# Optimization experiments

Hardware: AMD Instinct MI355X
Metric: run time of the kernel (lower is better)

## Reference

```python
import jax, jax.numpy as jnp
import numpy as np
from jax import lax


def setup_inputs() -> dict:
    key = jax.random.key(0)
    ks = jax.random.split(key, 20)
    B, T, Fin = 64, 360, 4
    C, H, W = 128, 32, 32          # encoder_hidden_dim, map size
    D, Hs, Ws = 128, 8, 8          # encoder_downsampled_dim, att feature map
    E, Hd, A, IF, O = 32, 128, 64, 128, 5
    IN = IF + C + E                # LSTMCell input size = 288
    s = 0.05
    # xy coords in [0, 0.31) so floor(v*100) is a valid index < 32
    prev_output_tokens = jax.random.uniform(ks[0], (B, T, Fin)) * 0.31 + 0.001
    feature = jax.random.normal(ks[1], (B, C, H, W))
    final_hidden = jax.random.normal(ks[2], (B, D, Hs, Ws))
    inp = dict(
        prev_output_tokens=prev_output_tokens,
        feature=feature,
        final_hidden=final_hidden,
        W_embed=jax.random.normal(ks[3], (Fin, E)) * s,
        b_embed=jnp.zeros((E,)),
        W_ih=jax.random.normal(ks[4], (IN, 4 * Hd)) * s,
        b_ih=jnp.zeros((4 * Hd,)),
        W_hh=jax.random.normal(ks[5], (Hd, 4 * Hd)) * s,
        b_hh=jnp.zeros((4 * Hd,)),
        W_h2att=jax.random.normal(ks[6], (Hd, A)) * s,
        b_h2att=jnp.zeros((A,)),
        W_alpha=jax.random.normal(ks[7], (A, 1)) * s,
        b_alpha=jnp.zeros((1,)),
        W_encproj=jax.random.normal(ks[8], (D, A)) * s,
        b_encproj=jnp.zeros((A,)),
        W_aap=jax.random.normal(ks[9], (Hd + D, IF)) * s,
        b_aap=jnp.zeros((IF,)),
        W_out=jax.random.normal(ks[10], (IF, O)) * s,
        b_out=jnp.zeros((O,)),
    )
    return inp


def reference(prev_output_tokens, feature, final_hidden,
              W_embed, b_embed, W_ih, b_ih, W_hh, b_hh,
              W_h2att, b_h2att, W_alpha, b_alpha,
              W_encproj, b_encproj, W_aap, b_aap, W_out, b_out):
    B, T, _ = prev_output_tokens.shape
    C, H = feature.shape[1], feature.shape[2]
    D = final_hidden.shape[1]
    Hd = W_hh.shape[0]
    IF = W_aap.shape[1]

    # embed_tokens (Linear)
    x_emb = prev_output_tokens @ W_embed + b_embed          # [B,T,E]

    # xy gather indices: floor(v*100), flat = y*H + x (torch uses size(-2))
    xy = (prev_output_tokens[..., :2] * 100).astype(jnp.int32)
    xy = jnp.where(xy == -1, 0, xy)
    idx = xy[..., 1] * H + xy[..., 0]                       # [B,T]
    feat_flat = feature.reshape(B, C, -1)                   # [B,C,H*W]

    # attention features and their projection (precomputed, as in torch)
    enc_feats = final_hidden.reshape(B, D, -1).transpose(0, 2, 1)   # [B,S,D]
    p_enc = enc_feats @ W_encproj + b_encproj                        # [B,S,A]

    def step(carry, xs):
        h, c, in_feed = carry
        xj, idxj = xs                                       # [B,E], [B]
        # gather encoder feature at the token's xy position
        in_seq = jnp.take_along_axis(feat_flat, idxj[:, None, None], axis=2)[..., 0]  # [B,C]
        inp = jnp.concatenate([xj, in_seq, in_feed], axis=-1)          # [B,288]
        # LSTMCell (torch gate order i,f,g,o)
        gates = inp @ W_ih + b_ih + h @ W_hh + b_hh
        i, f, g, o = jnp.split(gates, 4, axis=-1)
        c = jax.nn.sigmoid(f) * c + jax.nn.sigmoid(i) * jnp.tanh(g)
        h = jax.nn.sigmoid(o) * jnp.tanh(c)
        # additive attention
        att_h = h @ W_h2att + b_h2att                        # [B,A]
        dot = jnp.tanh(p_enc + att_h[:, None, :])            # [B,S,A]
        scores = (dot @ W_alpha)[..., 0] + b_alpha[0]        # [B,S]
        wgt = jax.nn.softmax(scores, axis=1)
        att_res = jnp.einsum('bs,bsd->bd', wgt, enc_feats)   # [B,D]
        out = jnp.concatenate([h, att_res], axis=-1) @ W_aap + b_aap  # [B,IF]
        return (h, c, out), out

    carry0 = (jnp.zeros((B, Hd), x_emb.dtype),
              jnp.zeros((B, Hd), x_emb.dtype),
              jnp.zeros((B, IF), x_emb.dtype))
    xs = (x_emb.transpose(1, 0, 2), idx.T)
    _, outs = lax.scan(step, carry0, xs)                     # [T,B,IF]
    x = outs.transpose(1, 0, 2)                              # [B,T,IF]
    return x @ W_out + b_out                                 # [B,T,5]
```

## Files before the change

### kernel.cpp

```cpp
#include <hip/hip_runtime.h>
#include <hip/hip_bf16.h>

#define BDIM 64
#define TDIM 360
#define BT (BDIM*TDIM)
#define CDIM 128
#define HWSZ 1024
#define SDIM 64
#define G4 512
#define KTOP 160

typedef __hip_bfloat16 bf16;

static __device__ __forceinline__ unsigned int f2bu(float x) {
    bf16 b = __float2bfloat16(x);
    unsigned short u; __builtin_memcpy(&u, &b, 2); return (unsigned int)u;
}
static __device__ __forceinline__ float b2f(bf16 x) { return __bfloat162float(x); }
static __device__ __forceinline__ float bl(unsigned int u) { return __uint_as_float(u << 16); }
static __device__ __forceinline__ float bh(unsigned int u) { return __uint_as_float(u & 0xffff0000u); }
static __device__ __forceinline__ float tanh_fast(float x) {
    float e = __expf(2.0f * x);
    return 1.0f - 2.0f / (e + 1.0f);
}
static __device__ __forceinline__ float sigm(float x) {
    return 1.0f / (1.0f + __expf(-x));
}

__device__ float        g_ArowsF[BT * KTOP];
__device__ float        g_pre2[BT * G4];
__device__ __align__(16) unsigned int g_wpk2[16 * 1024 * 4];
__device__ float        g_wrecA[128 * G4];
__device__ __align__(16) unsigned int g_encW2[BDIM * G4 * 32];
__device__ float        g_encWao[BDIM * 64 * 5];
__device__ float        g_penc[BDIM * SDIM * 64];
__device__ float        g_hw[BT * 192];
__device__ float        g_Wao[256 * 5];
__device__ float        g_bao[5];
__device__ float        g_bias[G4];
__device__ float        g_c0[G4];

__global__ void kA1(const float* __restrict__ tok, const float* __restrict__ feat,
                    const float* __restrict__ Wemb, const float* __restrict__ bemb) {
    int row  = blockIdx.x * 4 + (threadIdx.x >> 6);
    int lane = threadIdx.x & 63;
    const float* tp = tok + (size_t)row * 4;
    float t0 = tp[0], t1 = tp[1], t2 = tp[2], t3 = tp[3];
    int b = row / TDIM;
    int x = (int)(t0 * 100.0f);
    int y = (int)(t1 * 100.0f);
    x = min(max(x, 0), 31);
    y = min(max(y, 0), 31);
    int idx = y * 32 + x;
    float* out = g_ArowsF + (size_t)row * KTOP;
    if (lane < 32) {
        float e = t0 * Wemb[lane] + t1 * Wemb[32 + lane] +
                  t2 * Wemb[64 + lane] + t3 * Wemb[96 + lane] + bemb[lane];
        out[lane] = e;
    }
    const float* fb = feat + (size_t)b * CDIM * HWSZ + idx;
    out[32 + lane]      = fb[(size_t)lane * HWSZ];
    out[32 + 64 + lane] = fb[(size_t)(64 + lane) * HWSZ];
}

__global__ void kA2a(const float* __restrict__ Wih, const float* __restrict__ Whh,
                     const float* __restrict__ Waap) {
    __shared__ float sa0[128], sa1[128];
    int p = blockIdx.x, n = threadIdx.x;
    int r0 = 2 * p, r1 = 2 * p + 1;
    if (n < 128)            sa0[n]        = Waap[r0 * 128 + n];
    else if (n < 256)       sa1[n - 128]  = Waap[r1 * 128 + (n - 128)];
    __syncthreads();
    float acc0 = (r0 < 128) ? Whh[r0 * G4 + n] : 0.0f;
    float acc1 = (r1 < 128) ? Whh[r1 * G4 + n] : 0.0f;
    for (int j = 0; j < 128; ++j) {
        float wi = Wih[(160 + j) * G4 + n];
        acc0 += sa0[j] * wi;
        acc1 += sa1[j] * wi;
    }
    int kh = p >> 6, j = p & 63;
    int jblk = j >> 2, jj = j & 3;
    int u = kh * 512 + n;
    g_wpk2[((size_t)jblk * 1024 + u) * 4 + jj] = f2bu(acc0) | (f2bu(acc1) << 16);
    if (p >= 64) {
        g_wrecA[(r0 - 128) * G4 + n] = acc0;
        g_wrecA[(r1 - 128) * G4 + n] = acc1;
    }
}

__global__ void kA2c(const float* __restrict__ bih, const float* __restrict__ bhh,
                     const float* __restrict__ Wih, const float* __restrict__ Waap,
                     const float* __restrict__ baap, const float* __restrict__ Wout,
                     const float* __restrict__ bout) {
    __shared__ float sb[128];
    int n = threadIdx.x;
    if (n < 128) sb[n] = baap[n];
    __syncthreads();
    g_bias[n] = bih[n] + bhh[n];
    float c0 = 0.0f;
    for (int j = 0; j < 128; ++j) c0 += sb[j] * Wih[(160 + j) * G4 + n];
    g_c0[n] = c0;
    if (n < 256) {
        for (int o = 0; o < 5; ++o) {
            float acc = 0.0f;
            for (int j = 0; j < 128; ++j) acc += Waap[n * 128 + j] * Wout[j * 5 + o];
            g_Wao[n * 5 + o] = acc;
        }
    }
    if (n == 0) {
        for (int o = 0; o < 5; ++o) {
            float acc = bout[o];
            for (int j = 0; j < 128; ++j) acc += sb[j] * Wout[j * 5 + o];
            g_bao[o] = acc;
        }
    }
}

__global__ void kA2d(const float* __restrict__ FH, const float* __restrict__ Wep,
                     const float* __restrict__ bep) {
    __shared__ float sfh[128 * 64];
    int b = blockIdx.x, tid = threadIdx.x;
    for (int i = tid; i < 128 * 64; i += 256) sfh[i] = FH[(size_t)b * 128 * 64 + i];
    __syncthreads();
    int a = tid & 63, sg = tid >> 6;
    float bias = bep[a];
    float acc[16];
#pragma unroll
    for (int i = 0; i < 16; ++i) acc[i] = bias;
    for (int d = 0; d < 128; ++d) {
        float wa = Wep[d * 64 + a];
#pragma unroll
        for (int i = 0; i < 16; ++i) acc[i] += sfh[d * 64 + sg * 16 + i] * wa;
    }
    for (int i = 0; i < 16; ++i)
        g_penc[((size_t)b * 64 + sg * 16 + i) * 64 + a] = acc[i];
}

__global__ void kA2e(const float* __restrict__ FH) {
    __shared__ float encL[64][129];
    int b = blockIdx.x, tid = threadIdx.x;
    for (int i = tid; i < 8192; i += 512) {
        int d = i >> 6, s = i & 63;
        encL[s][d] = FH[(size_t)b * 8192 + i];
    }
    __syncthreads();
    int n = tid;
#pragma unroll 1
    for (int sc = 0; sc < 8; ++sc) {
        float acc[8];
#pragma unroll
        for (int j = 0; j < 8; ++j) acc[j] = 0.f;
        for (int d = 0; d < 128; ++d) {
            float wv = g_wrecA[d * G4 + n];
#pragma unroll
            for (int j = 0; j < 8; ++j) acc[j] += encL[sc * 8 + j][d] * wv;
        }
#pragma unroll
        for (int j = 0; j < 4; ++j) {
            int s2 = sc * 4 + j;
            g_encW2[((size_t)b * G4 + n) * 32 + s2] =
                f2bu(acc[2 * j]) | (f2bu(acc[2 * j + 1]) << 16);
        }
    }
    if (tid < 64) {
        for (int o = 0; o < 5; ++o) {
            float acc = 0.f;
            for (int d = 0; d < 128; ++d)
                acc += encL[tid][d] * g_Wao[(128 + d) * 5 + o];
            g_encWao[((size_t)b * 64 + tid) * 5 + o] = acc;
        }
    }
}

__global__ void __attribute__((amdgpu_flat_work_group_size(512, 512),
                               amdgpu_waves_per_eu(2, 2)))
kB(const float* __restrict__ Wih) {
    int n = threadIdx.x;
    int m0 = blockIdx.x * 8;
    int pl = ((n & 127) << 2) | (n >> 7);
    float racc[8];
#pragma unroll
    for (int r = 0; r < 8; ++r) racc[r] = 0.0f;
#pragma unroll 1
    for (int pass = 0; pass < 2; ++pass) {
        float wcol[80];
#pragma unroll
        for (int j = 0; j < 80; ++j) wcol[j] = Wih[(pass * 80 + j) * G4 + n];
#pragma unroll
        for (int r = 0; r < 8; ++r) {
            const float4* rp = (const float4*)(g_ArowsF + (size_t)(m0 + r) * KTOP + pass * 80);
            float a0 = 0.f, a1 = 0.f, a2 = 0.f, a3 = 0.f;
#pragma unroll
            for (int q = 0; q < 20; ++q) {
                float4 v = rp[q];
                a0 += wcol[4 * q + 0] * v.x;
                a1 += wcol[4 * q + 1] * v.y;
                a2 += wcol[4 * q + 2] * v.z;
                a3 += wcol[4 * q + 3] * v.w;
            }
            racc[r] += (a0 + a1) + (a2 + a3);
        }
    }
#pragma unroll
    for (int r = 0; r < 8; ++r)
        g_pre2[(size_t)(m0 + r) * G4 + pl] = racc[r];
}

#define CONS1(W, jb) { \
    float4 v0 = vals[2 * (jb)], v1 = vals[2 * (jb) + 1]; \
    acc0 += bl(W.x) * v0.x;  acc1 += bh(W.x) * v0.y; \
    acc0 += bl(W.y) * v0.z;  acc1 += bh(W.y) * v0.w; \
    acc0 += bl(W.z) * v1.x;  acc1 += bh(W.z) * v1.y; \
    acc0 += bl(W.w) * v1.z;  acc1 += bh(W.w) * v1.w; }
#define LDP(R, jb)  R = wp[(jb) * 1024];

#define SYNC() do { __builtin_amdgcn_sched_barrier(0); \
    asm volatile("s_waitcnt lgkmcnt(0)" ::: "memory"); \
    __builtin_amdgcn_s_barrier(); \
    __builtin_amdgcn_sched_barrier(0); } while (0)

__global__ void __launch_bounds__(512) kC(const float* __restrict__ Walpha,
                                          const float* __restrict__ balpha,
                                          const float* __restrict__ bh2a,
                                          const float* __restrict__ W2a) {
    __shared__ __align__(16) float s_h[128];
    __shared__ __align__(16) float s_atth[64];
    __shared__ float s_scores[64];
    __shared__ __align__(8)  float s_wgt[64];
    __shared__ float s_walpha[64];
    __shared__ float s_bh2a[64];
    extern __shared__ __align__(16) char dsm[];
    unsigned int* s_encW = (unsigned int*)dsm;
    float* s_penc = (float*)(dsm + 69632);
    bf16*  s_w2aT = (bf16*)(dsm + 69632 + 16640);

    int tid = threadIdx.x;
    int b = blockIdx.x;
    int lane = tid & 63;
    int qb = lane & ~3;
    int n = ((tid & 3) << 7) | (tid >> 2);
    int m = tid >> 2;

    const uint4* wp = ((const uint4*)g_wpk2) + n;
    uint4 P0,P1,P2,P3,P4,P5,P6,P7,P8,P9,P10,P11,P12,P13,P14,P15;
    LDP(P0,0)  LDP(P1,1)  LDP(P2,2)  LDP(P3,3)
    LDP(P4,4)  LDP(P5,5)  LDP(P6,6)  LDP(P7,7)
    LDP(P8,8)  LDP(P9,9)  LDP(P10,10) LDP(P11,11)
    LDP(P12,12) LDP(P13,13) LDP(P14,14) LDP(P15,15)

    float bias_r = g_bias[n];
    float bc_r   = bias_r + g_c0[n];
    float c_reg  = 0.0f;

    if (tid < 128) s_h[tid] = 0.0f;
    if (tid < 64) { s_walpha[tid] = Walpha[tid]; s_bh2a[tid] = bh2a[tid]; }
    for (int i = tid; i < 16384; i += 512) {
        int row = i >> 5, s2 = i & 31;
        int loc = ((row & 127) << 2) | (row >> 7);
        s_encW[loc * 34 + s2] = g_encW2[(size_t)b * 16384 + i];
    }
    for (int i = tid; i < 4096; i += 512) {
        int s = i >> 6, a = i & 63;
        s_penc[s * 65 + a] = g_penc[((size_t)b * 64 + s) * 64 + a];
    }
    for (int i = tid; i < 8192; i += 512) {
        int d = i >> 6, s = i & 63;
        s_w2aT[s * 136 + d] = __float2bfloat16(W2a[i]);
    }
    float bal = balpha[0];

    const float* pre2p = g_pre2 + (size_t)b * TDIM * G4 + tid;
    float* hwp0 = g_hw + (size_t)b * TDIM * 192;

    for (int t = 0; t < TDIM; ++t) {
        SYNC();
        float pre2v = pre2p[(size_t)t * G4];
        float acc0 = 0.f, acc1 = 0.f;
        const float4* vals = (const float4*)s_h;
        CONS1(P0,0)  CONS1(P1,1)  CONS1(P2,2)  CONS1(P3,3)
        CONS1(P4,4)  CONS1(P5,5)  CONS1(P6,6)  CONS1(P7,7)
        CONS1(P8,8)  CONS1(P9,9)  CONS1(P10,10) CONS1(P11,11)
        CONS1(P12,12) CONS1(P13,13) CONS1(P14,14) CONS1(P15,15)
        float g = acc0 + acc1 + pre2v + (t ? bc_r : bias_r);
        if (t) {
            const uint2* er = (const uint2*)(s_encW + tid * 34);
            const float2* wg2 = (const float2*)s_wgt;
            float w0 = 0.f, w1 = 0.f;
#pragma unroll
            for (int j = 0; j < 16; ++j) {
                uint2 ew = er[j];
                float2 wa = wg2[2 * j], wb = wg2[2 * j + 1];
                w0 += bl(ew.x) * wa.x;  w1 += bh(ew.x) * wa.y;
                w0 += bl(ew.y) * wb.x;  w1 += bh(ew.y) * wb.y;
            }
            g += w0 + w1;
        }
        {
            float gi = __shfl(g, qb + 0);
            float gf = __shfl(g, qb + 1);
            float gg = __shfl(g, qb + 2);
            float go = __shfl(g, qb + 3);
            float c = sigm(gf) * c_reg + sigm(gi) * tanh_fast(gg);
            c_reg = c;
            float h = sigm(go) * tanh_fast(c);
            if ((tid & 3) == 0) {
                s_h[m] = h;
                hwp0[(size_t)t * 192 + m] = h;
            }
        }
        SYNC();
        {
            int a = tid >> 3, sub = tid & 7;
            const float4* hv4 = (const float4*)s_h;
            float4 h0 = hv4[4 * sub], h1 = hv4[4 * sub + 1],
                   h2 = hv4[4 * sub + 2], h3 = hv4[4 * sub + 3];
            uint4 w0 = *(const uint4*)&s_w2aT[a * 136 + 16 * sub];
            uint4 w1 = *(const uint4*)&s_w2aT[a * 136 + 16 * sub + 8];
            float acc = bl(w0.x) * h0.x + bh(w0.x) * h0.y +
                        bl(w0.y) * h0.z + bh(w0.y) * h0.w +
                        bl(w0.z) * h1.x + bh(w0.z) * h1.y +
                        bl(w0.w) * h1.z + bh(w0.w) * h1.w +
                        bl(w1.x) * h2.x + bh(w1.x) * h2.y +
                        bl(w1.y) * h2.z + bh(w1.y) * h2.w +
                        bl(w1.z) * h3.x + bh(w1.z) * h3.y +
                        bl(w1.w) * h3.z + bh(w1.w) * h3.w;
            acc += __shfl_xor(acc, 1);
            acc += __shfl_xor(acc, 2);
            acc += __shfl_xor(acc, 4);
            if (sub == 0) s_atth[a] = acc + s_bh2a[a];
        }
        SYNC();
        {
            int ss = tid >> 3, sub = tid & 7;
            float acc = 0.f;
#pragma unroll
            for (int j = 0; j < 8; ++j) {
                int a = sub * 8 + j;
                float xv = s_penc[ss * 65 + a] + s_atth[a];
                acc += tanh_fast(xv) * s_walpha[a];
            }
            acc += __shfl_xor(acc, 1);
            acc += __shfl_xor(acc, 2);
            acc += __shfl_xor(acc, 4);
            if (sub == 0) s_scores[ss] = acc + bal;
        }
        SYNC();
        if (tid < 64) {
            float v = s_scores[tid];
            float mx = v;
#pragma unroll
            for (int off = 32; off > 0; off >>= 1) mx = fmaxf(mx, __shfl_xor(mx, off));
            float e = __expf(v - mx);
            float sum = e;
#pragma unroll
            for (int off = 32; off > 0; off >>= 1) sum += __shfl_xor(sum, off);
            float w = e / sum;
            s_wgt[tid] = w;
            hwp0[(size_t)t * 192 + 128 + tid] = w;
        }
    }
}

__global__ void kD(float* __restrict__ out) {
    int r = blockIdx.x * 4 + (threadIdx.x >> 6);
    int lane = threadIdx.x & 63;
    int b = r / TDIM;
    float acc[5] = {0.f, 0.f, 0.f, 0.f, 0.f};
    if (lane < 48) {
        const float4* hv = (const float4*)(g_hw + (size_t)r * 192);
        float4 v = hv[lane];
        int k0 = lane * 4;
        if (lane < 32) {
#pragma unroll
            for (int o = 0; o < 5; ++o)
                acc[o] = v.x * g_Wao[(k0 + 0) * 5 + o] + v.y * g_Wao[(k0 + 1) * 5 + o] +
                         v.z * g_Wao[(k0 + 2) * 5 + o] + v.w * g_Wao[(k0 + 3) * 5 + o];
        } else {
            int s0 = k0 - 128;
            const float* ew = g_encWao + ((size_t)b * 64 + s0) * 5;
#pragma unroll
            for (int o = 0; o < 5; ++o)
                acc[o] = v.x * ew[o] + v.y * ew[5 + o] + v.z * ew[10 + o] + v.w * ew[15 + o];
        }
    }
#pragma unroll
    for (int off = 32; off > 0; off >>= 1) {
#pragma unroll
        for (int o = 0; o < 5; ++o) acc[o] += __shfl_xor(acc[o], off);
    }
    if (lane == 0) {
#pragma unroll
        for (int o = 0; o < 5; ++o) out[(size_t)r * 5 + o] = acc[o] + g_bao[o];
    }
}

extern "C" void kernel_launch(void* const* d_in, const int* in_sizes, int n_in,
                              void* d_out, int out_size, void* d_ws, size_t ws_size,
                              hipStream_t stream) {
    (void)in_sizes; (void)n_in; (void)d_ws; (void)ws_size; (void)out_size;
    const float* tok  = (const float*)d_in[0];
    const float* feat = (const float*)d_in[1];
    const float* FH   = (const float*)d_in[2];
    const float* Wemb = (const float*)d_in[3];
    const float* bemb = (const float*)d_in[4];
    const float* Wih  = (const float*)d_in[5];
    const float* bih  = (const float*)d_in[6];
    const float* Whh  = (const float*)d_in[7];
    const float* bhh  = (const float*)d_in[8];
    const float* W2a  = (const float*)d_in[9];
    const float* bh2a = (const float*)d_in[10];
    const float* Wal  = (const float*)d_in[11];
    const float* bal  = (const float*)d_in[12];
    const float* Wep  = (const float*)d_in[13];
    const float* bep  = (const float*)d_in[14];
    const float* Waap = (const float*)d_in[15];
    const float* baap = (const float*)d_in[16];
    const float* Wout = (const float*)d_in[17];
    const float* bout = (const float*)d_in[18];
    float* out = (float*)d_out;

    const int kc_dyn_lds = 69632 + 16640 + 17408;
    (void)hipFuncSetAttribute((const void*)kC,
                              hipFuncAttributeMaxDynamicSharedMemorySize,
                              kc_dyn_lds);

    kA1<<<dim3(BT / 4), dim3(256), 0, stream>>>(tok, feat, Wemb, bemb);
    kA2a<<<dim3(128), dim3(512), 0, stream>>>(Wih, Whh, Waap);
    kA2c<<<dim3(1), dim3(512), 0, stream>>>(bih, bhh, Wih, Waap, baap, Wout, bout);
    kA2d<<<dim3(64), dim3(256), 0, stream>>>(FH, Wep, bep);
    kA2e<<<dim3(BDIM), dim3(512), 0, stream>>>(FH);
    kB<<<dim3(BT / 8), dim3(512), 0, stream>>>(Wih);
    kC<<<dim3(64), dim3(512), kc_dyn_lds, stream>>>(Wal, bal, bh2a, W2a);
    kD<<<dim3(BT / 4), dim3(256), 0, stream>>>(out);
}
```

Measured before the change: 1.459 ms.

## Switch recurrent matvecs to packed fp16 with v_dot2 instructions

Converts the packed recurrent weights, per-batch encoder weights, and h2att weights from bf16 to fp16 pairs. Hidden state and attention weights are also stored in shared memory as packed fp16 pairs. Inner products then use the fdot2 intrinsic, which does two multiply-adds per instruction, instead of unpacking bf16 and running scalar FMAs. This cuts ALU work and LDS traffic on the serial per-timestep critical path. In exchange, fp16 range and precision limits apply, the conversion uses round-toward-zero, and cross-lane shuffles are added to build the packed pairs.

Measured after the change: 1.328 ms. 1.1x faster.

```diff
diff --git a/kernel.cpp b/kernel.cpp
--- a/kernel.cpp
+++ b/kernel.cpp
@@ -11,14 +11,24 @@
 #define KTOP 160
 
 typedef __hip_bfloat16 bf16;
+typedef __fp16 h2 __attribute__((ext_vector_type(2)));
 
 static __device__ __forceinline__ unsigned int f2bu(float x) {
     bf16 b = __float2bfloat16(x);
     unsigned short u; __builtin_memcpy(&u, &b, 2); return (unsigned int)u;
 }
-static __device__ __forceinline__ float b2f(bf16 x) { return __bfloat162float(x); }
 static __device__ __forceinline__ float bl(unsigned int u) { return __uint_as_float(u << 16); }
 static __device__ __forceinline__ float bh(unsigned int u) { return __uint_as_float(u & 0xffff0000u); }
+static __device__ __forceinline__ h2 u2h(unsigned int u) {
+    h2 r; __builtin_memcpy(&r, &u, 4); return r;
+}
+static __device__ __forceinline__ unsigned int packh(float a, float b) {
+    h2 v = __builtin_amdgcn_cvt_pkrtz(a, b);
+    unsigned int u; __builtin_memcpy(&u, &v, 4); return u;
+}
+static __device__ __forceinline__ float fdot2(unsigned int a, unsigned int b, float c) {
+    return __builtin_amdgcn_fdot2(u2h(a), u2h(b), c, false);
+}
 static __device__ __forceinline__ float tanh_fast(float x) {
     float e = __expf(2.0f * x);
     return 1.0f - 2.0f / (e + 1.0f);
@@ -81,7 +91,7 @@
     int kh = p >> 6, j = p & 63;
     int jblk = j >> 2, jj = j & 3;
     int u = kh * 512 + n;
-    g_wpk2[((size_t)jblk * 1024 + u) * 4 + jj] = f2bu(acc0) | (f2bu(acc1) << 16);
+    g_wpk2[((size_t)jblk * 1024 + u) * 4 + jj] = packh(acc0, acc1);
     if (p >= 64) {
         g_wrecA[(r0 - 128) * G4 + n] = acc0;
         g_wrecA[(r1 - 128) * G4 + n] = acc1;
@@ -158,8 +168,7 @@
 #pragma unroll
         for (int j = 0; j < 4; ++j) {
             int s2 = sc * 4 + j;
-            g_encW2[((size_t)b * G4 + n) * 32 + s2] =
-                f2bu(acc[2 * j]) | (f2bu(acc[2 * j + 1]) << 16);
+            g_encW2[((size_t)b * G4 + n) * 32 + s2] = packh(acc[2 * j], acc[2 * j + 1]);
         }
     }
     if (tid < 64) {
@@ -206,12 +215,11 @@
         g_pre2[(size_t)(m0 + r) * G4 + pl] = racc[r];
 }
 
-#define CONS1(W, jb) { \
-    float4 v0 = vals[2 * (jb)], v1 = vals[2 * (jb) + 1]; \
-    acc0 += bl(W.x) * v0.x;  acc1 += bh(W.x) * v0.y; \
-    acc0 += bl(W.y) * v0.z;  acc1 += bh(W.y) * v0.w; \
-    acc0 += bl(W.z) * v1.x;  acc1 += bh(W.z) * v1.y; \
-    acc0 += bl(W.w) * v1.z;  acc1 += bh(W.w) * v1.w; }
+#define CONS1f(W, jb) { uint4 hp = hvals4[jb]; \
+    acc0 = fdot2(W.x, hp.x, acc0); \
+    acc1 = fdot2(W.y, hp.y, acc1); \
+    acc0 = fdot2(W.z, hp.z, acc0); \
+    acc1 = fdot2(W.w, hp.w, acc1); }
 #define LDP(R, jb)  R = wp[(jb) * 1024];
 
 #define SYNC() do { __builtin_amdgcn_sched_barrier(0); \
@@ -223,16 +231,16 @@
                                           const float* __restrict__ balpha,
                                           const float* __restrict__ bh2a,
                                           const float* __restrict__ W2a) {
-    __shared__ __align__(16) float s_h[128];
+    __shared__ __align__(16) unsigned int s_h2[64];
     __shared__ __align__(16) float s_atth[64];
     __shared__ float s_scores[64];
-    __shared__ __align__(8)  float s_wgt[64];
-    __shared__ float s_walpha[64];
+    __shared__ __align__(16) unsigned int s_wgt2[32];
+    __shared__ __align__(16) float s_walpha[64];
     __shared__ float s_bh2a[64];
     extern __shared__ __align__(16) char dsm[];
-    unsigned int* s_encW = (unsigned int*)dsm;
-    float* s_penc = (float*)(dsm + 69632);
-    bf16*  s_w2aT = (bf16*)(dsm + 69632 + 16640);
+    unsigned int* s_encW  = (unsigned int*)dsm;
+    float*        s_penc  = (float*)(dsm + 69632);
+    unsigned int* s_w2aTp = (unsigned int*)(dsm + 69632 + 16640);
 
     int tid = threadIdx.x;
     int b = blockIdx.x;
@@ -252,8 +260,7 @@
     float bc_r   = bias_r + g_c0[n];
     float c_reg  = 0.0f;
 
-    if (tid < 128) s_h[tid] = 0.0f;
-    if (tid < 64) { s_walpha[tid] = Walpha[tid]; s_bh2a[tid] = bh2a[tid]; }
+    if (tid < 64) { s_h2[tid] = 0u; s_walpha[tid] = Walpha[tid]; s_bh2a[tid] = bh2a[tid]; }
     for (int i = tid; i < 16384; i += 512) {
         int row = i >> 5, s2 = i & 31;
         int loc = ((row & 127) << 2) | (row >> 7);
@@ -263,9 +270,9 @@
         int s = i >> 6, a = i & 63;
         s_penc[s * 65 + a] = g_penc[((size_t)b * 64 + s) * 64 + a];
     }
-    for (int i = tid; i < 8192; i += 512) {
-        int d = i >> 6, s = i & 63;
-        s_w2aT[s * 136 + d] = __float2bfloat16(W2a[i]);
+    for (int i = tid; i < 4096; i += 512) {
+        int a = i & 63, k2 = i >> 6;
+        s_w2aTp[a * 68 + k2] = packh(W2a[(2 * k2) * 64 + a], W2a[(2 * k2 + 1) * 64 + a]);
     }
     float bal = balpha[0];
 
@@ -276,22 +283,21 @@
         SYNC();
         float pre2v = pre2p[(size_t)t * G4];
         float acc0 = 0.f, acc1 = 0.f;
-        const float4* vals = (const float4*)s_h;
-        CONS1(P0,0)  CONS1(P1,1)  CONS1(P2,2)  CONS1(P3,3)
-        CONS1(P4,4)  CONS1(P5,5)  CONS1(P6,6)  CONS1(P7,7)
-        CONS1(P8,8)  CONS1(P9,9)  CONS1(P10,10) CONS1(P11,11)
-        CONS1(P12,12) CONS1(P13,13) CONS1(P14,14) CONS1(P15,15)
+        const uint4* hvals4 = (const uint4*)s_h2;
+        CONS1f(P0,0)  CONS1f(P1,1)  CONS1f(P2,2)  CONS1f(P3,3)
+        CONS1f(P4,4)  CONS1f(P5,5)  CONS1f(P6,6)  CONS1f(P7,7)
+        CONS1f(P8,8)  CONS1f(P9,9)  CONS1f(P10,10) CONS1f(P11,11)
+        CONS1f(P12,12) CONS1f(P13,13) CONS1f(P14,14) CONS1f(P15,15)
         float g = acc0 + acc1 + pre2v + (t ? bc_r : bias_r);
         if (t) {
             const uint2* er = (const uint2*)(s_encW + tid * 34);
-            const float2* wg2 = (const float2*)s_wgt;
+            const uint2* wg = (const uint2*)s_wgt2;
             float w0 = 0.f, w1 = 0.f;
 #pragma unroll
             for (int j = 0; j < 16; ++j) {
-                uint2 ew = er[j];
-                float2 wa = wg2[2 * j], wb = wg2[2 * j + 1];
-                w0 += bl(ew.x) * wa.x;  w1 += bh(ew.x) * wa.y;
-                w0 += bl(ew.y) * wb.x;  w1 += bh(ew.y) * wb.y;
+                uint2 ew = er[j], ww = wg[j];
+                w0 = fdot2(ew.x, ww.x, w0);
+                w1 = fdot2(ew.y, ww.y, w1);
             }
             g += w0 + w1;
         }
@@ -303,27 +309,23 @@
             float c = sigm(gf) * c_reg + sigm(gi) * tanh_fast(gg);
             c_reg = c;
             float h = sigm(go) * tanh_fast(c);
-            if ((tid & 3) == 0) {
-                s_h[m] = h;
-                hwp0[(size_t)t * 192 + m] = h;
-            }
+            if ((tid & 3) == 0) hwp0[(size_t)t * 192 + m] = h;
+            float h_p = __shfl(h, lane ^ 4);
+            if ((tid & 7) == 0) s_h2[tid >> 3] = packh(h, h_p);
         }
         SYNC();
         {
             int a = tid >> 3, sub = tid & 7;
-            const float4* hv4 = (const float4*)s_h;
-            float4 h0 = hv4[4 * sub], h1 = hv4[4 * sub + 1],
-                   h2 = hv4[4 * sub + 2], h3 = hv4[4 * sub + 3];
-            uint4 w0 = *(const uint4*)&s_w2aT[a * 136 + 16 * sub];
-            uint4 w1 = *(const uint4*)&s_w2aT[a * 136 + 16 * sub + 8];
-            float acc = bl(w0.x) * h0.x + bh(w0.x) * h0.y +
-                        bl(w0.y) * h0.z + bh(w0.y) * h0.w +
-                        bl(w0.z) * h1.x + bh(w0.z) * h1.y +
-                        bl(w0.w) * h1.z + bh(w0.w) * h1.w +
-                        bl(w1.x) * h2.x + bh(w1.x) * h2.y +
-                        bl(w1.y) * h2.z + bh(w1.y) * h2.w +
-                        bl(w1.z) * h3.x + bh(w1.z) * h3.y +
-                        bl(w1.w) * h3.z + bh(w1.w) * h3.w;
+            const uint4* hv = (const uint4*)s_h2;
+            uint4 hA = hv[2 * sub], hB = hv[2 * sub + 1];
+            const uint4* wr = (const uint4*)(s_w2aTp + a * 68 + 8 * sub);
+            uint4 wA = wr[0], wB = wr[1];
+            float a0 = 0.f, a1 = 0.f;
+            a0 = fdot2(wA.x, hA.x, a0);  a1 = fdot2(wA.y, hA.y, a1);
+            a0 = fdot2(wA.z, hA.z, a0);  a1 = fdot2(wA.w, hA.w, a1);
+            a0 = fdot2(wB.x, hB.x, a0);  a1 = fdot2(wB.y, hB.y, a1);
+            a0 = fdot2(wB.z, hB.z, a0);  a1 = fdot2(wB.w, hB.w, a1);
+            float acc = a0 + a1;
             acc += __shfl_xor(acc, 1);
             acc += __shfl_xor(acc, 2);
             acc += __shfl_xor(acc, 4);
@@ -355,8 +357,9 @@
 #pragma unroll
             for (int off = 32; off > 0; off >>= 1) sum += __shfl_xor(sum, off);
             float w = e / sum;
-            s_wgt[tid] = w;
             hwp0[(size_t)t * 192 + 128 + tid] = w;
+            float w_p = __shfl(w, lane ^ 1);
+            if ((tid & 1) == 0) s_wgt2[tid >> 1] = packh(w, w_p);
         }
     }
 }
```
